# Performance work log

Measured on AMD Instinct MI355X. Metric: run time of the kernel, lower is better.

Reference implementation:

```python
import jax, jax.numpy as jnp
import numpy as np
from jax import lax

DIM = 8            # per-head dim
GROUPS = 192       # 3 * heads, groups of the pointwise aggreg conv
EPS_ATT = 1e-15
EPS_BN = 1e-5


def conv1x1(x, w):
    # x: (B,C,H,W), w: (O,C)
    return jnp.einsum('bchw,oc->bohw', x, w)


def setup_inputs() -> dict:
    key = jax.random.key(0)
    ks = jax.random.split(key, 9)
    B, C, H, W = 4, 512, 64, 64
    td3 = 3 * 512  # 3 * total_dim = 1536
    return {
        'x':       jax.random.normal(ks[0], (B, C, H, W), jnp.float32),
        'w_qkv':   jax.random.normal(ks[1], (td3, C), jnp.float32) * 0.05,
        'w_dw':    jax.random.normal(ks[2], (td3, 1, 5, 5), jnp.float32) * 0.05,
        'w_pw':    jax.random.normal(ks[3], (GROUPS, 8, 8), jnp.float32) * 0.05,
        'w_proj':  jax.random.normal(ks[4], (512, 1024), jnp.float32) * 0.05,
        'bn_gamma': 1.0 + 0.1 * jax.random.normal(ks[5], (512,), jnp.float32),
        'bn_beta': 0.1 * jax.random.normal(ks[6], (512,), jnp.float32),
        'bn_mean': 0.1 * jax.random.normal(ks[7], (512,), jnp.float32),
        'bn_var':  0.5 + jax.random.uniform(ks[8], (512,), jnp.float32),
    }


def reference(x, w_qkv, w_dw, w_pw, w_proj, bn_gamma, bn_beta, bn_mean, bn_var):
    B, _, H, W = x.shape
    # qkv 1x1 conv (no norm / act)
    qkv = conv1x1(x, w_qkv)                      # (B,1536,H,W)
    # multi-scale aggreg branch: depthwise 5x5 then grouped 1x1
    y = lax.conv_general_dilated(
        qkv, w_dw, window_strides=(1, 1), padding=((2, 2), (2, 2)),
        feature_group_count=qkv.shape[1],
        dimension_numbers=('NCHW', 'OIHW', 'NCHW'))
    yg = y.reshape(B, GROUPS, 8, H, W)
    y = jnp.einsum('bgihw,goi->bgohw', yg, w_pw).reshape(B, -1, H, W)
    ms = jnp.concatenate([qkv, y], axis=1)       # (B,3072,H,W)

    # relu linear attention (fp32)
    N = H * W
    t = ms.astype(jnp.float32).reshape(B, -1, 3 * DIM, N)   # (B,128,24,N)
    q = jax.nn.relu(t[:, :, :DIM])               # (B,h,8,N)
    k = jax.nn.relu(t[:, :, DIM:2 * DIM])        # (B,h,8,N)
    v = t[:, :, 2 * DIM:]                        # (B,h,8,N)
    v = jnp.concatenate([v, jnp.ones_like(v[:, :, :1])], axis=2)  # (B,h,9,N)
    vk = jnp.einsum('bhdn,bhen->bhde', v, k)     # (B,h,9,8)
    out = jnp.einsum('bhde,bhen->bhdn', vk, q)   # (B,h,9,N)
    out = out[:, :, :DIM] / (out[:, :, DIM:] + EPS_ATT)
    out = out.reshape(B, -1, H, W).astype(ms.dtype)  # (B,1024,H,W)

    # proj 1x1 conv + BatchNorm2d (inference, running stats)
    p = conv1x1(out, w_proj)                     # (B,512,H,W)
    scale = (bn_gamma / jnp.sqrt(bn_var + EPS_BN))[None, :, None, None]
    shift = (bn_beta - bn_mean * bn_gamma / jnp.sqrt(bn_var + EPS_BN))[None, :, None, None]
    return p * scale + shift
```

## Files before the change

kernel.cpp:

```cpp
#include <hip/hip_runtime.h>
#include <cstddef>


#define NPIX 4096
#define TD3 1536

typedef _Float16 f16;
typedef __attribute__((ext_vector_type(8))) _Float16 v8h;
typedef __attribute__((ext_vector_type(4))) float v4f;
typedef unsigned short ushort_t;

#define GLL16(g, l) __builtin_amdgcn_global_load_lds(                         \
    (const __attribute__((address_space(1))) unsigned int*)(g),               \
    (__attribute__((address_space(3))) unsigned int*)(l), 16, 0, 0)

template <int SPLITB, int BN>
__global__ __launch_bounds__(256) void gemm_f16(
    const f16* __restrict__ Ah, const f16* __restrict__ Al,
    const f16* __restrict__ Bh, const f16* __restrict__ Bl,
    float* __restrict__ C, int M, int N, int K,
    const float* __restrict__ bn_g, const float* __restrict__ bn_b,
    const float* __restrict__ bn_m, const float* __restrict__ bn_v)
{
    __shared__ f16 AsH[128 * 32];
    __shared__ f16 AsL[128 * 32];
    __shared__ f16 BsH[128 * 32];
    __shared__ f16 BsL[SPLITB ? 128 * 32 : 64];

    const int tid  = threadIdx.x;
    const int lane = tid & 63;
    const int w    = tid >> 6;
    const int wm   = w >> 1, wn = w & 1;
    const int mBase = blockIdx.y * 128, nBase = blockIdx.x * 128;
    Bh += (size_t)blockIdx.z * N * K;
    if (SPLITB) Bl += (size_t)blockIdx.z * N * K;
    C  += (size_t)blockIdx.z * M * N;

    const f16* gAh[2]; const f16* gAl[2]; const f16* gBh[2]; const f16* gBl[2];
    int ldsOff[2];
    #pragma unroll
    for (int p = 0; p < 2; ++p) {
        int off = (w * 2 + p) * 1024 + lane * 16;
        int r  = off >> 6;
        int ci = (off & 63) >> 1;
        gAh[p] = Ah + (size_t)(mBase + r) * K + ci;
        gAl[p] = Al + (size_t)(mBase + r) * K + ci;
        gBh[p] = Bh + (size_t)(nBase + r) * K + ci;
        if (SPLITB) gBl[p] = Bl + (size_t)(nBase + r) * K + ci;
        ldsOff[p] = (w * 2 + p) * 512;
    }

    v4f acc[4][4];
    #pragma unroll
    for (int i = 0; i < 4; ++i)
        #pragma unroll
        for (int j = 0; j < 4; ++j)
            acc[i][j] = (v4f){0.f, 0.f, 0.f, 0.f};

    const int kq = lane >> 4;
    const int rm = lane & 15;
    const int KT = K >> 5;
    for (int kt = 0; kt < KT; ++kt) {
        #pragma unroll
        for (int p = 0; p < 2; ++p) {
            GLL16(gAh[p] + kt * 32, &AsH[ldsOff[p]]);
            GLL16(gAl[p] + kt * 32, &AsL[ldsOff[p]]);
            GLL16(gBh[p] + kt * 32, &BsH[ldsOff[p]]);
            if (SPLITB) GLL16(gBl[p] + kt * 32, &BsL[ldsOff[p]]);
        }
        __syncthreads();

        v8h ah[4], al[4], bh[4], bl[4];
        #pragma unroll
        for (int i = 0; i < 4; ++i) {
            ah[i] = *(const v8h*)&AsH[(wm * 64 + i * 16 + rm) * 32 + kq * 8];
            al[i] = *(const v8h*)&AsL[(wm * 64 + i * 16 + rm) * 32 + kq * 8];
            bh[i] = *(const v8h*)&BsH[(wn * 64 + i * 16 + rm) * 32 + kq * 8];
            if (SPLITB)
                bl[i] = *(const v8h*)&BsL[(wn * 64 + i * 16 + rm) * 32 + kq * 8];
        }
        #pragma unroll
        for (int i = 0; i < 4; ++i)
            #pragma unroll
            for (int j = 0; j < 4; ++j) {
                acc[i][j] = __builtin_amdgcn_mfma_f32_16x16x32_f16(
                    ah[i], bh[j], acc[i][j], 0, 0, 0);
                acc[i][j] = __builtin_amdgcn_mfma_f32_16x16x32_f16(
                    al[i], bh[j], acc[i][j], 0, 0, 0);
                if (SPLITB)
                    acc[i][j] = __builtin_amdgcn_mfma_f32_16x16x32_f16(
                        ah[i], bl[j], acc[i][j], 0, 0, 0);
            }
        __syncthreads();
    }

    const int rq = lane >> 4, cn = lane & 15;
    #pragma unroll
    for (int i = 0; i < 4; ++i) {
        #pragma unroll
        for (int rg = 0; rg < 4; ++rg) {
            int row = mBase + wm * 64 + i * 16 + rq * 4 + rg;
            float sc = 1.f, sh = 0.f;
            if (BN) {
                sc = bn_g[row] * rsqrtf(bn_v[row] + 1e-5f);
                sh = bn_b[row] - bn_m[row] * sc;
            }
            #pragma unroll
            for (int j = 0; j < 4; ++j) {
                int col = nBase + wn * 64 + j * 16 + cn;
                float v = acc[i][j][rg];
                C[(size_t)row * N + col] = BN ? (v * sc + sh) : v;
            }
        }
    }
}

__global__ __launch_bounds__(256) void cvt_split(
    const float* __restrict__ src, f16* __restrict__ dh, f16* __restrict__ dl,
    int n4)
{
    int i = blockIdx.x * 256 + threadIdx.x;
    if (i < n4) {
        float4 f = ((const float4*)src)[i];
        f16 h[4], l[4];
        float ff[4] = {f.x, f.y, f.z, f.w};
        #pragma unroll
        for (int q = 0; q < 4; ++q) {
            h[q] = (f16)ff[q];
            l[q] = (f16)(ff[q] - (float)h[q]);
        }
        *(uint2*)&dh[(size_t)i * 4] = *(uint2*)h;
        *(uint2*)&dl[(size_t)i * 4] = *(uint2*)l;
    }
}

__global__ __launch_bounds__(256) void transp_split(
    const float* __restrict__ src, f16* __restrict__ dh, f16* __restrict__ dl)
{
    __shared__ float t[64][65];
    const int tid = threadIdx.x;
    const int n0 = blockIdx.x * 64, c0 = blockIdx.y * 64, b = blockIdx.z;

    const int row = tid >> 2;
    const int nn  = (tid & 3) * 16;
    const float* sp = src + ((size_t)b * 512 + c0 + row) * NPIX + n0 + nn;
    #pragma unroll
    for (int q = 0; q < 4; ++q) {
        float4 f = *(const float4*)(sp + q * 4);
        t[row][nn + q * 4 + 0] = f.x;
        t[row][nn + q * 4 + 1] = f.y;
        t[row][nn + q * 4 + 2] = f.z;
        t[row][nn + q * 4 + 3] = f.w;
    }
    __syncthreads();

    const int nrow = tid >> 2;
    const int cc   = (tid & 3) * 16;
    f16 h[16], l[16];
    #pragma unroll
    for (int q = 0; q < 16; ++q) {
        float f = t[cc + q][nrow];
        h[q] = (f16)f;
        l[q] = (f16)(f - (float)h[q]);
    }
    size_t di = ((size_t)b * NPIX + n0 + nrow) * 512 + c0 + cc;
    *(uint4*)&dh[di] = *(uint4*)&h[0];
    *(uint4*)&dh[di + 8] = *(uint4*)&h[8];
    *(uint4*)&dl[di] = *(uint4*)&l[0];
    *(uint4*)&dl[di + 8] = *(uint4*)&l[8];
}

__global__ __launch_bounds__(256) void dwpw(
    const float* __restrict__ qkv, const float* __restrict__ w_dw,
    const float* __restrict__ w_pw, float* __restrict__ y)
{
    __shared__ float tile[8][8][68];
    __shared__ float wd[8][25];
    __shared__ float wp[64];

    const int tid = threadIdx.x;
    const int g = blockIdx.y;
    const int b = blockIdx.z;
    const int h0 = blockIdx.x * 4;
    const size_t cbase = (size_t)b * TD3 + g * 8;

    if (tid < 200) wd[tid / 25][tid % 25] = w_dw[(g * 8 + tid / 25) * 25 + tid % 25];
    if (tid >= 192) wp[tid - 192] = w_pw[g * 64 + (tid - 192)];

    #pragma unroll
    for (int it = 0; it < 17; ++it) {
        int idx = tid + it * 256;
        int ch = idx / 544;
        int rem = idx - ch * 544;
        int r = rem / 68;
        int cc = rem - r * 68;
        int gh = h0 + r - 2, gw = cc - 2;
        float v = 0.f;
        if (gh >= 0 && gh < 64 && gw >= 0 && gw < 64)
            v = qkv[(cbase + ch) * NPIX + gh * 64 + gw];
        tile[ch][r][cc] = v;
    }
    __syncthreads();

    const int r = tid >> 6;
    const int wc = tid & 63;
    float dwv[8];
    #pragma unroll
    for (int i = 0; i < 8; ++i) {
        float s = 0.f;
        #pragma unroll
        for (int di = 0; di < 5; ++di)
            #pragma unroll
            for (int dj = 0; dj < 5; ++dj)
                s = fmaf(tile[i][r + di][wc + dj], wd[i][di * 5 + dj], s);
        dwv[i] = s;
    }
    #pragma unroll
    for (int o = 0; o < 8; ++o) {
        float s = 0.f;
        #pragma unroll
        for (int i = 0; i < 8; ++i) s = fmaf(dwv[i], wp[o * 8 + i], s);
        y[(cbase + o) * NPIX + (h0 + r) * 64 + wc] = s;
    }
}

__global__ __launch_bounds__(256) void attn_stats(
    const float* __restrict__ qkv, const float* __restrict__ yy,
    float* __restrict__ vkout)
{
    const int h = blockIdx.x;
    const int b = blockIdx.y;
    const float* src = (h < 64)
        ? qkv + ((size_t)b * TD3 + h * 24) * NPIX
        : yy  + ((size_t)b * TD3 + (h - 64) * 24) * NPIX;

    float acc[9][8];
    #pragma unroll
    for (int d = 0; d < 9; ++d)
        #pragma unroll
        for (int e = 0; e < 8; ++e) acc[d][e] = 0.f;

    for (int n = threadIdx.x; n < NPIX; n += 256) {
        float kr[8], vv[8];
        #pragma unroll
        for (int e = 0; e < 8; ++e) kr[e] = fmaxf(src[(8 + e) * NPIX + n], 0.f);
        #pragma unroll
        for (int d = 0; d < 8; ++d) vv[d] = src[(16 + d) * NPIX + n];
        #pragma unroll
        for (int d = 0; d < 8; ++d)
            #pragma unroll
            for (int e = 0; e < 8; ++e) acc[d][e] = fmaf(vv[d], kr[e], acc[d][e]);
        #pragma unroll
        for (int e = 0; e < 8; ++e) acc[8][e] += kr[e];
    }

    __shared__ float part[4][72];
    const int lane = threadIdx.x & 63, wave = threadIdx.x >> 6;
    #pragma unroll
    for (int i = 0; i < 72; ++i) {
        float v = acc[i / 8][i % 8];
        #pragma unroll
        for (int off = 32; off; off >>= 1) v += __shfl_down(v, off, 64);
        if (lane == 0) part[wave][i] = v;
    }
    __syncthreads();
    if (threadIdx.x < 72) {
        float v = part[0][threadIdx.x] + part[1][threadIdx.x] +
                  part[2][threadIdx.x] + part[3][threadIdx.x];
        vkout[((size_t)b * 128 + h) * 72 + threadIdx.x] = v;
    }
}

__global__ __launch_bounds__(256) void attn_apply_t(
    const float* __restrict__ qkv, const float* __restrict__ yy,
    const float* __restrict__ vkin, f16* __restrict__ attout)
{
    const int h = blockIdx.y;
    const int b = blockIdx.z;
    const int n = blockIdx.x * 256 + threadIdx.x;

    __shared__ float vk[72];
    if (threadIdx.x < 72)
        vk[threadIdx.x] = vkin[((size_t)b * 128 + h) * 72 + threadIdx.x];
    __syncthreads();

    const float* src = (h < 64)
        ? qkv + ((size_t)b * TD3 + h * 24) * NPIX
        : yy  + ((size_t)b * TD3 + (h - 64) * 24) * NPIX;

    float qr[8];
    #pragma unroll
    for (int e = 0; e < 8; ++e) qr[e] = fmaxf(src[e * NPIX + n], 0.f);

    float den = 0.f;
    #pragma unroll
    for (int e = 0; e < 8; ++e) den = fmaf(vk[64 + e], qr[e], den);
    float inv = 1.f / (den + 1e-15f);

    f16 o[8];
    #pragma unroll
    for (int d = 0; d < 8; ++d) {
        float num = 0.f;
        #pragma unroll
        for (int e = 0; e < 8; ++e) num = fmaf(vk[d * 8 + e], qr[e], num);
        o[d] = (f16)(num * inv);
    }
    *(uint4*)&attout[((size_t)b * NPIX + n) * 1024 + h * 8] = *(uint4*)o;
}

extern "C" void kernel_launch(void* const* d_in, const int* in_sizes, int n_in,
                              void* d_out, int out_size, void* d_ws, size_t ws_size,
                              hipStream_t stream)
{
    (void)in_sizes; (void)n_in; (void)out_size; (void)ws_size;
    const float* x      = (const float*)d_in[0];
    const float* w_qkv  = (const float*)d_in[1];
    const float* w_dw   = (const float*)d_in[2];
    const float* w_pw   = (const float*)d_in[3];
    const float* w_proj = (const float*)d_in[4];
    const float* bn_g   = (const float*)d_in[5];
    const float* bn_b   = (const float*)d_in[6];
    const float* bn_m   = (const float*)d_in[7];
    const float* bn_v   = (const float*)d_in[8];
    float* out = (float*)d_out;

    char* ws = (char*)d_ws;
    float* qkv     = (float*)(ws);
    float* y       = (float*)(ws + 100663296);
    f16*   x_t_h   = (f16*)(ws + 201326592);
    f16*   x_t_l   = (f16*)(ws + 218103808);
    f16*   attout  = (f16*)(ws + 201326592);
    f16*   w_qkv_h = (f16*)(ws + 234881024);
    f16*   w_qkv_l = (f16*)(ws + 236453888);
    f16*   w_proj_h= (f16*)(ws + 238026752);
    f16*   w_proj_l= (f16*)(ws + 239075328);
    float* vk      = out;

    cvt_split<<<768, 256, 0, stream>>>(w_qkv, w_qkv_h, w_qkv_l, 196608);
    cvt_split<<<512, 256, 0, stream>>>(w_proj, w_proj_h, w_proj_l, 131072);
    transp_split<<<dim3(64, 8, 4), 256, 0, stream>>>(x, x_t_h, x_t_l);
    gemm_f16<1, 0><<<dim3(32, 12, 4), 256, 0, stream>>>(
        w_qkv_h, w_qkv_l, x_t_h, x_t_l, qkv, 1536, 4096, 512,
        nullptr, nullptr, nullptr, nullptr);
    dwpw<<<dim3(16, 192, 4), 256, 0, stream>>>(qkv, w_dw, w_pw, y);
    attn_stats<<<dim3(128, 4), 256, 0, stream>>>(qkv, y, vk);
    attn_apply_t<<<dim3(16, 128, 4), 256, 0, stream>>>(qkv, y, vk, attout);
    gemm_f16<0, 1><<<dim3(32, 4, 4), 256, 0, stream>>>(
        w_proj_h, w_proj_l, attout, nullptr, out, 512, 4096, 1024,
        bn_g, bn_b, bn_m, bn_v);
}
```

Baseline: 359.9 us.

## Enlarge dwpw row tile and compute four output pixels per thread

The depthwise+pointwise kernel now processes 16 rows per block instead of 4, which cuts the halo overhead from 8 loaded rows per 4 output rows to 20 per 16. Each thread computes four adjacent pixels from a sliding window read with float4 shared loads, reusing each loaded value across several taps, and writes float4 outputs. The trade-off is more registers per thread, a 4x smaller grid (3072 blocks), and a larger shared-memory tile that may lower occupancy.

```diff
diff --git a/kernel.cpp b/kernel.cpp
--- a/kernel.cpp
+++ b/kernel.cpp
@@ -174,53 +174,70 @@
     const float* __restrict__ qkv, const float* __restrict__ w_dw,
     const float* __restrict__ w_pw, float* __restrict__ y)
 {
-    __shared__ float tile[8][8][68];
+    __shared__ float tile[8][20][68];
     __shared__ float wd[8][25];
     __shared__ float wp[64];
 
     const int tid = threadIdx.x;
     const int g = blockIdx.y;
     const int b = blockIdx.z;
-    const int h0 = blockIdx.x * 4;
+    const int h0 = blockIdx.x * 16;
     const size_t cbase = (size_t)b * TD3 + g * 8;
 
     if (tid < 200) wd[tid / 25][tid % 25] = w_dw[(g * 8 + tid / 25) * 25 + tid % 25];
     if (tid >= 192) wp[tid - 192] = w_pw[g * 64 + (tid - 192)];
 
-    #pragma unroll
-    for (int it = 0; it < 17; ++it) {
+    for (int it = 0; it < 43; ++it) {
         int idx = tid + it * 256;
-        int ch = idx / 544;
-        int rem = idx - ch * 544;
-        int r = rem / 68;
-        int cc = rem - r * 68;
-        int gh = h0 + r - 2, gw = cc - 2;
-        float v = 0.f;
-        if (gh >= 0 && gh < 64 && gw >= 0 && gw < 64)
-            v = qkv[(cbase + ch) * NPIX + gh * 64 + gw];
-        tile[ch][r][cc] = v;
+        if (idx < 10880) {
+            int ch = idx / 1360;
+            int rem = idx - ch * 1360;
+            int rr = rem / 68;
+            int cc = rem - rr * 68;
+            int gh = h0 + rr - 2, gw = cc - 2;
+            float v = 0.f;
+            if (gh >= 0 && gh < 64 && gw >= 0 && gw < 64)
+                v = qkv[(cbase + ch) * NPIX + gh * 64 + gw];
+            tile[ch][rr][cc] = v;
+        }
     }
     __syncthreads();
 
-    const int r = tid >> 6;
-    const int wc = tid & 63;
-    float dwv[8];
+    const int r  = tid >> 4;
+    const int wc = tid & 15;
+    float dwv[8][4];
     #pragma unroll
     for (int i = 0; i < 8; ++i) {
-        float s = 0.f;
-        #pragma unroll
-        for (int di = 0; di < 5; ++di)
+        float s0 = 0.f, s1 = 0.f, s2 = 0.f, s3 = 0.f;
+        #pragma unroll
+        for (int di = 0; di < 5; ++di) {
+            const float* rp = &tile[i][r + di][wc * 4];
+            float4 lo = *(const float4*)rp;
+            float4 hi = *(const float4*)(rp + 4);
+            float win[8] = {lo.x, lo.y, lo.z, lo.w, hi.x, hi.y, hi.z, hi.w};
             #pragma unroll
-            for (int dj = 0; dj < 5; ++dj)
-                s = fmaf(tile[i][r + di][wc + dj], wd[i][di * 5 + dj], s);
-        dwv[i] = s;
+            for (int dj = 0; dj < 5; ++dj) {
+                float wgt = wd[i][di * 5 + dj];
+                s0 = fmaf(win[dj + 0], wgt, s0);
+                s1 = fmaf(win[dj + 1], wgt, s1);
+                s2 = fmaf(win[dj + 2], wgt, s2);
+                s3 = fmaf(win[dj + 3], wgt, s3);
+            }
+        }
+        dwv[i][0] = s0; dwv[i][1] = s1; dwv[i][2] = s2; dwv[i][3] = s3;
     }
     #pragma unroll
     for (int o = 0; o < 8; ++o) {
-        float s = 0.f;
-        #pragma unroll
-        for (int i = 0; i < 8; ++i) s = fmaf(dwv[i], wp[o * 8 + i], s);
-        y[(cbase + o) * NPIX + (h0 + r) * 64 + wc] = s;
+        float4 s = {0.f, 0.f, 0.f, 0.f};
+        #pragma unroll
+        for (int i = 0; i < 8; ++i) {
+            float wgt = wp[o * 8 + i];
+            s.x = fmaf(dwv[i][0], wgt, s.x);
+            s.y = fmaf(dwv[i][1], wgt, s.y);
+            s.z = fmaf(dwv[i][2], wgt, s.z);
+            s.w = fmaf(dwv[i][3], wgt, s.w);
+        }
+        *(float4*)&y[(cbase + o) * NPIX + (h0 + r) * 64 + wc * 4] = s;
     }
 }
 
@@ -342,7 +359,7 @@
     gemm_f16<1, 0><<<dim3(32, 12, 4), 256, 0, stream>>>(
         w_qkv_h, w_qkv_l, x_t_h, x_t_l, qkv, 1536, 4096, 512,
         nullptr, nullptr, nullptr, nullptr);
-    dwpw<<<dim3(16, 192, 4), 256, 0, stream>>>(qkv, w_dw, w_pw, y);
+    dwpw<<<dim3(4, 192, 4), 256, 0, stream>>>(qkv, w_dw, w_pw, y);
     attn_stats<<<dim3(128, 4), 256, 0, stream>>>(qkv, y, vk);
     attn_apply_t<<<dim3(16, 128, 4), 256, 0, stream>>>(qkv, y, vk, attout);
     gemm_f16<0, 1><<<dim3(32, 4, 4), 256, 0, stream>>>(
```

After: 401.8 us. 11.6% more time.

## Fuse attention stats and apply kernels into one per-head kernel

Applied to the files above, without the earlier changes.

Merges the vk reduction kernel and the attention apply kernel so each block computes its head's vk matrix in shared memory, then loops over all pixels to produce the output. This removes one launch and the global round-trip of vk. The apply phase now runs on only 512 blocks instead of 8192, and each thread loops over 16 pixels with 72 vk values held in registers. That cuts parallelism and raises register pressure.

```diff
diff --git a/kernel.cpp b/kernel.cpp
--- a/kernel.cpp
+++ b/kernel.cpp
@@ -224,9 +224,9 @@
     }
 }
 
-__global__ __launch_bounds__(256) void attn_stats(
+__global__ __launch_bounds__(256) void attn_fused(
     const float* __restrict__ qkv, const float* __restrict__ yy,
-    float* __restrict__ vkout)
+    f16* __restrict__ attout)
 {
     const int h = blockIdx.x;
     const int b = blockIdx.y;
@@ -255,6 +255,7 @@
     }
 
     __shared__ float part[4][72];
+    __shared__ float vks[72];
     const int lane = threadIdx.x & 63, wave = threadIdx.x >> 6;
     #pragma unroll
     for (int i = 0; i < 72; ++i) {
@@ -264,48 +265,33 @@
         if (lane == 0) part[wave][i] = v;
     }
     __syncthreads();
-    if (threadIdx.x < 72) {
-        float v = part[0][threadIdx.x] + part[1][threadIdx.x] +
-                  part[2][threadIdx.x] + part[3][threadIdx.x];
-        vkout[((size_t)b * 128 + h) * 72 + threadIdx.x] = v;
-    }
-}
-
-__global__ __launch_bounds__(256) void attn_apply_t(
-    const float* __restrict__ qkv, const float* __restrict__ yy,
-    const float* __restrict__ vkin, f16* __restrict__ attout)
-{
-    const int h = blockIdx.y;
-    const int b = blockIdx.z;
-    const int n = blockIdx.x * 256 + threadIdx.x;
-
-    __shared__ float vk[72];
     if (threadIdx.x < 72)
-        vk[threadIdx.x] = vkin[((size_t)b * 128 + h) * 72 + threadIdx.x];
+        vks[threadIdx.x] = part[0][threadIdx.x] + part[1][threadIdx.x] +
+                           part[2][threadIdx.x] + part[3][threadIdx.x];
     __syncthreads();
 
-    const float* src = (h < 64)
-        ? qkv + ((size_t)b * TD3 + h * 24) * NPIX
-        : yy  + ((size_t)b * TD3 + (h - 64) * 24) * NPIX;
-
-    float qr[8];
-    #pragma unroll
-    for (int e = 0; e < 8; ++e) qr[e] = fmaxf(src[e * NPIX + n], 0.f);
-
-    float den = 0.f;
-    #pragma unroll
-    for (int e = 0; e < 8; ++e) den = fmaf(vk[64 + e], qr[e], den);
-    float inv = 1.f / (den + 1e-15f);
-
-    f16 o[8];
-    #pragma unroll
-    for (int d = 0; d < 8; ++d) {
-        float num = 0.f;
-        #pragma unroll
-        for (int e = 0; e < 8; ++e) num = fmaf(vk[d * 8 + e], qr[e], num);
-        o[d] = (f16)(num * inv);
-    }
-    *(uint4*)&attout[((size_t)b * NPIX + n) * 1024 + h * 8] = *(uint4*)o;
+    float vkr[72];
+    #pragma unroll
+    for (int i = 0; i < 72; ++i) vkr[i] = vks[i];
+
+    for (int n = threadIdx.x; n < NPIX; n += 256) {
+        float qr[8];
+        #pragma unroll
+        for (int e = 0; e < 8; ++e) qr[e] = fmaxf(src[e * NPIX + n], 0.f);
+        float den = 0.f;
+        #pragma unroll
+        for (int e = 0; e < 8; ++e) den = fmaf(vkr[64 + e], qr[e], den);
+        float inv = 1.f / (den + 1e-15f);
+        f16 o[8];
+        #pragma unroll
+        for (int d = 0; d < 8; ++d) {
+            float num = 0.f;
+            #pragma unroll
+            for (int e = 0; e < 8; ++e) num = fmaf(vkr[d * 8 + e], qr[e], num);
+            o[d] = (f16)(num * inv);
+        }
+        *(uint4*)&attout[((size_t)b * NPIX + n) * 1024 + h * 8] = *(uint4*)o;
+    }
 }
 
 extern "C" void kernel_launch(void* const* d_in, const int* in_sizes, int n_in,
@@ -334,7 +320,6 @@
     f16*   w_qkv_l = (f16*)(ws + 236453888);
     f16*   w_proj_h= (f16*)(ws + 238026752);
     f16*   w_proj_l= (f16*)(ws + 239075328);
-    float* vk      = out;
 
     cvt_split<<<768, 256, 0, stream>>>(w_qkv, w_qkv_h, w_qkv_l, 196608);
     cvt_split<<<512, 256, 0, stream>>>(w_proj, w_proj_h, w_proj_l, 131072);
@@ -343,8 +328,7 @@
         w_qkv_h, w_qkv_l, x_t_h, x_t_l, qkv, 1536, 4096, 512,
         nullptr, nullptr, nullptr, nullptr);
     dwpw<<<dim3(16, 192, 4), 256, 0, stream>>>(qkv, w_dw, w_pw, y);
-    attn_stats<<<dim3(128, 4), 256, 0, stream>>>(qkv, y, vk);
-    attn_apply_t<<<dim3(16, 128, 4), 256, 0, stream>>>(qkv, y, vk, attout);
+    attn_fused<<<dim3(128, 4), 256, 0, stream>>>(qkv, y, attout);
     gemm_f16<0, 1><<<dim3(32, 4, 4), 256, 0, stream>>>(
         w_proj_h, w_proj_l, attout, nullptr, out, 512, 4096, 1024,
         bn_g, bn_b, bn_m, bn_v);
```

Result: slower. 459.3 us (+27.6%).
